# Optimization experiments

Hardware: AMD Instinct MI355X
Metric: run time of the kernel (lower is better)

Reference implementation:

```python
import jax, jax.numpy as jnp
import numpy as np

N_NODES = 25000
N_EDGES = 50000
NUM_ATOMS = 26
HID = 64
EMB = 64
N_GRAPHS = 64
NUM_NN_ITER = 3


def setup_inputs() -> dict:
    key = jax.random.key(0)
    ks = jax.random.split(key, 16)

    def nrm(k, shape, s=0.1):
        return jax.random.normal(k, shape, dtype=jnp.float32) * s

    x = jax.random.uniform(ks[0], (N_NODES, NUM_ATOMS), dtype=jnp.float32)
    edge_index = jax.random.randint(ks[1], (2, N_EDGES), 0, N_NODES)
    edge_attr = jax.random.uniform(ks[2], (N_EDGES, 4), dtype=jnp.float32)
    batch = jnp.sort(jax.random.randint(ks[3], (N_NODES,), 0, N_GRAPHS))

    params = dict(
        W_in=nrm(ks[4], (NUM_ATOMS, HID)), b_in=jnp.zeros((HID,), jnp.float32),
        We1=nrm(ks[5], (4, 128)), be1=jnp.zeros((128,), jnp.float32),
        We2=nrm(ks[6], (128, HID * HID), 0.02), be2=jnp.zeros((HID * HID,), jnp.float32),
        W_root=nrm(ks[7], (HID, HID)), b_conv=jnp.zeros((HID,), jnp.float32),
        W_ih=nrm(ks[8], (3 * HID, HID)), b_ih=jnp.zeros((3 * HID,), jnp.float32),
        W_hh=nrm(ks[9], (3 * HID, HID)), b_hh=jnp.zeros((3 * HID,), jnp.float32),
        Wo1=nrm(ks[10], (HID, HID)), bo1=jnp.zeros((HID,), jnp.float32),
        Wo2=nrm(ks[11], (HID, EMB)), bo2=jnp.zeros((EMB,), jnp.float32),
        Wp=nrm(ks[12], (EMB + NUM_ATOMS, 1)), bp=jnp.zeros((1,), jnp.float32),
    )
    return {"x": x, "edge_index": edge_index, "edge_attr": edge_attr, "batch": batch, **params}


def reference(x, edge_index, edge_attr, batch,
              W_in, b_in, We1, be1, We2, be2, W_root, b_conv,
              W_ih, b_ih, W_hh, b_hh, Wo1, bo1, Wo2, bo2, Wp, bp):
    src, dst = edge_index[0], edge_index[1]
    # edge MLP -> per-edge (HID, HID) weight blocks; edge_attr is fixed so compute once
    Wedge = (jax.nn.relu(edge_attr @ We1 + be1) @ We2 + be2).reshape(-1, HID, HID)  # (E, h, h)

    out = jax.nn.relu(x @ W_in + b_in)  # (N, h)
    h = out
    for _ in range(NUM_NN_ITER):
        # NNConv (aggr='add'): root transform + gather->bmm->scatter_add
        msg = jnp.einsum('ei,eio->eo', out[src], Wedge)           # (E, h)
        agg = jax.ops.segment_sum(msg, dst, num_segments=N_NODES)  # (N, h)
        m = jax.nn.relu(out @ W_root + agg + b_conv)
        # single-step GRU cell (torch GRU equations)
        gi = m @ W_ih.T + b_ih
        gh = h @ W_hh.T + b_hh
        i_r, i_z, i_n = jnp.split(gi, 3, axis=-1)
        h_r, h_z, h_n = jnp.split(gh, 3, axis=-1)
        r = jax.nn.sigmoid(i_r + h_r)
        z = jax.nn.sigmoid(i_z + h_z)
        n = jnp.tanh(i_n + r * h_n)
        h = (1.0 - z) * n + z * h
        out = h

    o = jax.nn.relu(out @ Wo1 + bo1) @ Wo2 + bo2            # (N, EMB)
    feat = jnp.concatenate([o, x], axis=1)                  # (N, EMB + NUM_ATOMS)
    # F.normalize: row-wise L2 with eps clamp
    feat = feat / jnp.maximum(jnp.linalg.norm(feat, axis=1, keepdims=True), 1e-12)
    # scatter_mean readout over graphs
    cnt = jax.ops.segment_sum(jnp.ones((N_NODES,), jnp.float32), batch, num_segments=N_GRAPHS)
    readout = jax.ops.segment_sum(feat, batch, num_segments=N_GRAPHS) / jnp.maximum(cnt, 1.0)[:, None]
    ratio = jax.nn.sigmoid(readout @ Wp + bp)               # (G, 1)
    return feat, ratio
```

## Files before the change

### kernel.cpp

```cpp
#include <hip/hip_runtime.h>
#include <math.h>

#define NN 25000
#define NE 50000
#define NEP2 50176
#define NBLK 196
#define NATOM 26
#define NUM_ITER 3
#define NCH 33
#define NPB 32

typedef __attribute__((ext_vector_type(8))) short bf16x8;
typedef __attribute__((ext_vector_type(8))) unsigned short ushort8_t;
typedef __attribute__((ext_vector_type(4))) float f32x4;
union FragU { bf16x8 v; ushort4 q[2]; };

static __device__ __forceinline__ ushort f2bf(float f) {
  unsigned u = __float_as_uint(f);
  unsigned r = (u + 0x7FFFu + ((u >> 16) & 1u)) >> 16;
  return (ushort)r;
}
static __device__ __forceinline__ unsigned cvt_pk_bf16(float a, float b) {
  unsigned r;
  asm("v_cvt_pk_bf16_f32 %0, %1, %2" : "=v"(r) : "v"(a), "v"(b));
  return r;
}
static __device__ __forceinline__ float bflo(unsigned u) { return __uint_as_float(u << 16); }
static __device__ __forceinline__ float bfhi(unsigned u) { return __uint_as_float(u & 0xFFFF0000u); }

__global__ __launch_bounds__(256) void edge_mlp_pack_kernel(
    const float* __restrict__ ea, const float* __restrict__ We1,
    const float* __restrict__ be1, ushort* __restrict__ Upkt) {
  int t = threadIdx.x;
  int el = t & 63, seg = t >> 6;
  int e = blockIdx.x * 64 + el;
  bool valid = (e < NE);
  float a0 = 0.f, a1 = 0.f, a2 = 0.f, a3 = 0.f;
  if (valid) { a0 = ea[e * 4]; a1 = ea[e * 4 + 1]; a2 = ea[e * 4 + 2]; a3 = ea[e * 4 + 3]; }
  #pragma unroll
  for (int q = 0; q < 8; ++q) {
    int g = seg * 8 + q;
    ushort out[4];
    #pragma unroll
    for (int kk = 0; kk < 4; ++kk) {
      int k = g * 4 + kk;
      float v = be1[k];
      v = fmaf(a0, We1[k], v);
      v = fmaf(a1, We1[128 + k], v);
      v = fmaf(a2, We1[256 + k], v);
      v = fmaf(a3, We1[384 + k], v);
      out[kk] = valid ? f2bf(fmaxf(v, 0.f)) : (ushort)0;
    }
    *(ushort4*)&Upkt[((size_t)g * NEP2 + e) * 4] = *(ushort4*)out;
  }
  if (seg == 0) {
    ushort out[4] = {(ushort)(valid ? 0x3F80 : 0), 0, 0, 0};
    *(ushort4*)&Upkt[((size_t)32 * NEP2 + e) * 4] = *(ushort4*)out;
  }
}

__global__ __launch_bounds__(256) void bpk_pack_kernel(
    const float* __restrict__ We2, const float* __restrict__ be2,
    ushort* __restrict__ Bpk) {
  int idx = blockIdx.x * 256 + threadIdx.x;
  int lane = idx & 63;
  int nt = (idx >> 6) & 3;
  int ks = (idx >> 8) & 7;
  int c = idx >> 11;
  int l15 = lane & 15, lg = lane >> 4;
  int o = nt * 16 + l15;
  ushort v[8];
  #pragma unroll
  for (int j = 0; j < 8; ++j) {
    int kl = (j < 4) ? (4 * lg + j) : (12 + 4 * lg + j);
    int f = c * 256 + ks * 32 + kl;
    int k = f >> 6, i = f & 63;
    float wv = 0.f;
    if (k < 128) wv = We2[(size_t)k * 4096 + i * 64 + o];
    else if (k == 128) wv = be2[i * 64 + o];
    v[j] = f2bf(wv);
  }
  *(ushort8_t*)(Bpk + (size_t)idx * 8) = *(ushort8_t*)v;
}

__global__ __launch_bounds__(256) void nw_pack_kernel(
    const float* __restrict__ W_root, const float* __restrict__ W_ih,
    const float* __restrict__ W_hh, ushort* __restrict__ Wr_pk,
    ushort* __restrict__ Bih_pk, ushort* __restrict__ Bhh_pk) {
  int idx = blockIdx.x * 256 + threadIdx.x;
  if (idx >= 3584) return;
  int lane, nt, ks, kind;
  ushort* dstp;
  if (idx < 512)      { kind = 0; int f = idx;        lane = f & 63; nt = (f >> 6) % 4;  ks = (f >> 6) / 4;  dstp = Wr_pk  + (size_t)f * 8; }
  else if (idx < 2048){ kind = 1; int f = idx - 512;  lane = f & 63; nt = (f >> 6) % 12; ks = (f >> 6) / 12; dstp = Bih_pk + (size_t)f * 8; }
  else                { kind = 2; int f = idx - 2048; lane = f & 63; nt = (f >> 6) % 12; ks = (f >> 6) / 12; dstp = Bhh_pk + (size_t)f * 8; }
  int l15 = lane & 15, lg = lane >> 4;
  int col = nt * 16 + l15;
  ushort v[8];
  #pragma unroll
  for (int j = 0; j < 8; ++j) {
    int kl = (j < 4) ? (4 * lg + j) : (12 + 4 * lg + j);
    int i = ks * 32 + kl;
    float wv;
    if (kind == 0)      wv = W_root[i * 64 + col];
    else if (kind == 1) wv = W_ih[col * 64 + i];
    else                wv = W_hh[col * 64 + i];
    v[j] = f2bf(wv);
  }
  *(ushort8_t*)dstp = *(ushort8_t*)v;
}

__global__ __launch_bounds__(512, 1) void edge_rgemm_kernel(
    const ushort* __restrict__ Upkt, const ushort* __restrict__ Bpk,
    const float* __restrict__ hv, const int* __restrict__ src,
    const int* __restrict__ dst, float* __restrict__ agg) {
  __shared__ ushort sB[2][16384];
  __shared__ ushort sU[2][1024];
  __shared__ ushort sS[256][72];
  int tid = threadIdx.x;
  int lane = tid & 63, w = tid >> 6;
  int l15 = lane & 15, lg = lane >> 4;
  int e0 = blockIdx.x * 256;

  #pragma unroll
  for (int r = 0; r < 8; ++r) {
    int idx = r * 512 + tid;
    int el = idx >> 4, part = idx & 15;
    int e = e0 + el;
    float4 v = make_float4(0.f, 0.f, 0.f, 0.f);
    if (e < NE) v = ((const float4*)hv)[(size_t)src[e] * 16 + part];
    unsigned lo = cvt_pk_bf16(v.x, v.y);
    unsigned hi = cvt_pk_bf16(v.z, v.w);
    *(uint2*)&sS[el][part * 4] = make_uint2(lo, hi);
  }

  ushort8_t rB[4]; uint2 rU;
  #pragma unroll
  for (int r = 0; r < 4; ++r)
    rB[r] = *(const ushort8_t*)(Bpk + ((size_t)r * 512 + tid) * 8);
  if (tid < 256) rU = *(const uint2*)(Upkt + (size_t)e0 * 4 + tid * 4);
  #pragma unroll
  for (int r = 0; r < 4; ++r)
    *(ushort8_t*)&sB[0][((size_t)r * 512 + tid) * 8] = rB[r];
  if (tid < 256) *(uint2*)&sU[0][tid * 4] = rU;
  __syncthreads();

  float4 sreg[2][2][2];
  #pragma unroll
  for (int mt = 0; mt < 2; ++mt)
    #pragma unroll
    for (int p = 0; p < 2; ++p)
      #pragma unroll
      for (int g = 0; g < 2; ++g) {
        uint2 d = *(const uint2*)&sS[w * 32 + mt * 16 + l15][p * 32 + g * 16 + 4 * lg];
        sreg[mt][p][g] = make_float4(bflo(d.x), bfhi(d.x), bflo(d.y), bfhi(d.y));
      }

  f32x4 acc[2][4];
  #pragma unroll
  for (int mt = 0; mt < 2; ++mt)
    #pragma unroll
    for (int nt = 0; nt < 4; ++nt) acc[mt][nt] = (f32x4){0.f, 0.f, 0.f, 0.f};

  for (int c = 0; c < NCH; ++c) {
    int cur = c & 1;
    bool more = (c + 1 < NCH);
    if (more) {
      const ushort* bs = Bpk + (size_t)(c + 1) * 16384;
      #pragma unroll
      for (int r = 0; r < 4; ++r)
        rB[r] = *(const ushort8_t*)(bs + ((size_t)r * 512 + tid) * 8);
      if (tid < 256)
        rU = *(const uint2*)(Upkt + ((size_t)(c + 1) * NEP2 + e0) * 4 + tid * 4);
    }
    float uu[2][4];
    #pragma unroll
    for (int mt = 0; mt < 2; ++mt) {
      uint2 d = *(const uint2*)&sU[cur][(w * 32 + mt * 16 + l15) * 4];
      uu[mt][0] = bflo(d.x); uu[mt][1] = bfhi(d.x);
      uu[mt][2] = bflo(d.y); uu[mt][3] = bfhi(d.y);
    }
    #pragma unroll
    for (int ks = 0; ks < 8; ++ks) {
      int p = ks & 1, ku = ks >> 1;
      bf16x8 bfr[4];
      #pragma unroll
      for (int nt = 0; nt < 4; ++nt)
        bfr[nt] = *(const bf16x8*)&sB[cur][(((size_t)ks * 4 + nt) * 64 + lane) * 8];
      #pragma unroll
      for (int mt = 0; mt < 2; ++mt) {
        float u = uu[mt][ku];
        float4 s0 = sreg[mt][p][0], s1 = sreg[mt][p][1];
        union { bf16x8 v; unsigned u32[4]; } af;
        af.u32[0] = cvt_pk_bf16(s0.x * u, s0.y * u);
        af.u32[1] = cvt_pk_bf16(s0.z * u, s0.w * u);
        af.u32[2] = cvt_pk_bf16(s1.x * u, s1.y * u);
        af.u32[3] = cvt_pk_bf16(s1.z * u, s1.w * u);
        #pragma unroll
        for (int nt = 0; nt < 4; ++nt)
          acc[mt][nt] = __builtin_amdgcn_mfma_f32_16x16x32_bf16(af.v, bfr[nt], acc[mt][nt], 0, 0, 0);
      }
    }
    if (more) {
      int nb = cur ^ 1;
      #pragma unroll
      for (int r = 0; r < 4; ++r)
        *(ushort8_t*)&sB[nb][((size_t)r * 512 + tid) * 8] = rB[r];
      if (tid < 256) *(uint2*)&sU[nb][tid * 4] = rU;
    }
    __syncthreads();
  }

  #pragma unroll
  for (int mt = 0; mt < 2; ++mt) {
    #pragma unroll
    for (int rr = 0; rr < 4; ++rr) {
      int e = e0 + w * 32 + mt * 16 + lg * 4 + rr;
      if (e < NE) {
        int d = dst[e];
        #pragma unroll
        for (int nt = 0; nt < 4; ++nt)
          atomicAdd(&agg[(size_t)d * 64 + nt * 16 + l15], acc[mt][nt][rr]);
      }
    }
  }
}

__global__ __launch_bounds__(256) void node_in_kernel(
    const float* __restrict__ x, const float* __restrict__ W_in,
    const float* __restrict__ b_in, float* __restrict__ h) {
  int idx = blockIdx.x * 256 + threadIdx.x;
  if (idx >= NN * 64) return;
  int n = idx >> 6, c = idx & 63;
  float acc = b_in[c];
  #pragma unroll
  for (int j = 0; j < NATOM; ++j) acc = fmaf(x[n * NATOM + j], W_in[j * 64 + c], acc);
  h[idx] = fmaxf(acc, 0.f);
}

__global__ __launch_bounds__(256, 1) void node_update2_kernel(
    float* __restrict__ hv, const float* __restrict__ agg,
    const ushort* __restrict__ Wr_pk, const ushort* __restrict__ Bih_pk,
    const ushort* __restrict__ Bhh_pk, const float* __restrict__ b_conv,
    const float* __restrict__ b_ih, const float* __restrict__ b_hh) {
  __shared__ ushort h_lds[128][72];
  __shared__ ushort m_lds[128][72];
  int tid = threadIdx.x;
  int lane = tid & 63, w = tid >> 6;
  int l15 = lane & 15, lg = lane >> 4;
  int n0 = blockIdx.x * 128;

  #pragma unroll
  for (int r = 0; r < 8; ++r) {
    int idx = r * 256 + tid;
    int row = idx >> 4, part = idx & 15;
    int n = n0 + row;
    float4 v = make_float4(0.f, 0.f, 0.f, 0.f);
    if (n < NN) v = ((const float4*)hv)[(size_t)n * 16 + part];
    *(uint2*)&h_lds[row][part * 4] =
        make_uint2(cvt_pk_bf16(v.x, v.y), cvt_pk_bf16(v.z, v.w));
  }
  __syncthreads();

  bf16x8 ah[2][2];
  #pragma unroll
  for (int mt = 0; mt < 2; ++mt)
    #pragma unroll
    for (int ks = 0; ks < 2; ++ks) {
      int row = w * 32 + mt * 16 + l15;
      FragU f;
      f.q[0] = *(const ushort4*)&h_lds[row][ks * 32 + 4 * lg];
      f.q[1] = *(const ushort4*)&h_lds[row][ks * 32 + 16 + 4 * lg];
      ah[mt][ks] = f.v;
    }

  f32x4 accm[2][4];
  #pragma unroll
  for (int mt = 0; mt < 2; ++mt)
    #pragma unroll
    for (int nt = 0; nt < 4; ++nt) accm[mt][nt] = (f32x4){0.f, 0.f, 0.f, 0.f};
  #pragma unroll
  for (int ks = 0; ks < 2; ++ks)
    #pragma unroll
    for (int nt = 0; nt < 4; ++nt) {
      bf16x8 b = *(const bf16x8*)(Wr_pk + ((size_t)((ks * 4 + nt) * 64 + lane)) * 8);
      #pragma unroll
      for (int mt = 0; mt < 2; ++mt)
        accm[mt][nt] = __builtin_amdgcn_mfma_f32_16x16x32_bf16(ah[mt][ks], b, accm[mt][nt], 0, 0, 0);
    }
  #pragma unroll
  for (int mt = 0; mt < 2; ++mt)
    #pragma unroll
    for (int nt = 0; nt < 4; ++nt) {
      int col = nt * 16 + l15;
      float bc = b_conv[col];
      #pragma unroll
      for (int rr = 0; rr < 4; ++rr) {
        int row = w * 32 + mt * 16 + lg * 4 + rr;
        int n = n0 + row;
        float val = 0.f;
        if (n < NN) val = fmaxf(accm[mt][nt][rr] + agg[(size_t)n * 64 + col] + bc, 0.f);
        m_lds[row][col] = f2bf(val);
      }
    }
  __syncthreads();

  bf16x8 am[2][2];
  #pragma unroll
  for (int mt = 0; mt < 2; ++mt)
    #pragma unroll
    for (int ks = 0; ks < 2; ++ks) {
      int row = w * 32 + mt * 16 + l15;
      FragU f;
      f.q[0] = *(const ushort4*)&m_lds[row][ks * 32 + 4 * lg];
      f.q[1] = *(const ushort4*)&m_lds[row][ks * 32 + 16 + 4 * lg];
      am[mt][ks] = f.v;
    }

  f32x4 acc_s[2][8], acc_in[2][4], acc_hn[2][4];
  #pragma unroll
  for (int mt = 0; mt < 2; ++mt) {
    #pragma unroll
    for (int nt = 0; nt < 8; ++nt) acc_s[mt][nt] = (f32x4){0.f, 0.f, 0.f, 0.f};
    #pragma unroll
    for (int nt = 0; nt < 4; ++nt) {
      acc_in[mt][nt] = (f32x4){0.f, 0.f, 0.f, 0.f};
      acc_hn[mt][nt] = (f32x4){0.f, 0.f, 0.f, 0.f};
    }
  }
  #pragma unroll
  for (int ks = 0; ks < 2; ++ks) {
    #pragma unroll
    for (int nt = 0; nt < 8; ++nt) {
      bf16x8 bi = *(const bf16x8*)(Bih_pk + ((size_t)((ks * 12 + nt) * 64 + lane)) * 8);
      bf16x8 bh = *(const bf16x8*)(Bhh_pk + ((size_t)((ks * 12 + nt) * 64 + lane)) * 8);
      #pragma unroll
      for (int mt = 0; mt < 2; ++mt) {
        acc_s[mt][nt] = __builtin_amdgcn_mfma_f32_16x16x32_bf16(am[mt][ks], bi, acc_s[mt][nt], 0, 0, 0);
        acc_s[mt][nt] = __builtin_amdgcn_mfma_f32_16x16x32_bf16(ah[mt][ks], bh, acc_s[mt][nt], 0, 0, 0);
      }
    }
    #pragma unroll
    for (int nt = 8; nt < 12; ++nt) {
      bf16x8 bi = *(const bf16x8*)(Bih_pk + ((size_t)((ks * 12 + nt) * 64 + lane)) * 8);
      bf16x8 bh = *(const bf16x8*)(Bhh_pk + ((size_t)((ks * 12 + nt) * 64 + lane)) * 8);
      #pragma unroll
      for (int mt = 0; mt < 2; ++mt) {
        acc_in[mt][nt - 8] = __builtin_amdgcn_mfma_f32_16x16x32_bf16(am[mt][ks], bi, acc_in[mt][nt - 8], 0, 0, 0);
        acc_hn[mt][nt - 8] = __builtin_amdgcn_mfma_f32_16x16x32_bf16(ah[mt][ks], bh, acc_hn[mt][nt - 8], 0, 0, 0);
      }
    }
  }

  #pragma unroll
  for (int mt = 0; mt < 2; ++mt)
    #pragma unroll
    for (int nt = 0; nt < 4; ++nt) {
      int col = nt * 16 + l15;
      float b_sr = b_ih[col] + b_hh[col];
      float b_sz = b_ih[64 + col] + b_hh[64 + col];
      float b_in_ = b_ih[128 + col];
      float b_hn = b_hh[128 + col];
      #pragma unroll
      for (int rr = 0; rr < 4; ++rr) {
        int row = w * 32 + mt * 16 + lg * 4 + rr;
        int n = n0 + row;
        if (n >= NN) continue;
        float Sr = acc_s[mt][nt][rr] + b_sr;
        float Sz = acc_s[mt][nt + 4][rr] + b_sz;
        float vin = acc_in[mt][nt][rr] + b_in_;
        float vhn = acc_hn[mt][nt][rr] + b_hn;
        float r = 1.f / (1.f + __expf(-Sr));
        float z = 1.f / (1.f + __expf(-Sz));
        float nn = tanhf(fmaf(r, vhn, vin));
        float hp = hv[(size_t)n * 64 + col];
        hv[(size_t)n * 64 + col] = (1.f - z) * nn + z * hp;
      }
    }
}

__global__ __launch_bounds__(256) void head2_kernel(
    const float* __restrict__ hv, const float* __restrict__ x,
    const float* __restrict__ Wo1, const float* __restrict__ bo1,
    const float* __restrict__ Wo2, const float* __restrict__ bo2,
    float* __restrict__ feat) {
  __shared__ float wo1[64 * 64];
  __shared__ float wo2[64 * 64];
  __shared__ float s_row[NPB * 64];
  __shared__ float s_o1[NPB * 64];
  int tid = threadIdx.x;
  int n0 = blockIdx.x * NPB;

  for (int idx = tid; idx < 64 * 16; idx += 256) {
    ((float4*)wo1)[idx] = ((const float4*)Wo1)[idx];
    ((float4*)wo2)[idx] = ((const float4*)Wo2)[idx];
  }
  for (int idx = tid; idx < NPB * 64; idx += 256) {
    int n = n0 + (idx >> 6);
    s_row[idx] = (n < NN) ? hv[(size_t)n * 64 + (idx & 63)] : 0.f;
  }
  __syncthreads();

  int c = tid & 63, g = tid >> 6;
  #pragma unroll
  for (int q = 0; q < 8; ++q) {
    int nl = g + 4 * q;
    float a = bo1[c];
    for (int i = 0; i < 64; ++i) a = fmaf(s_row[nl * 64 + i], wo1[i * 64 + c], a);
    s_o1[nl * 64 + c] = fmaxf(a, 0.f);
  }
  __syncthreads();
  #pragma unroll
  for (int q = 0; q < 8; ++q) {
    int nl = g + 4 * q;
    int n = n0 + nl;
    float b = bo2[c];
    for (int i = 0; i < 64; ++i) b = fmaf(s_o1[nl * 64 + i], wo2[i * 64 + c], b);
    float xv = (c < NATOM && n < NN) ? x[(size_t)n * NATOM + c] : 0.f;
    float sq = b * b + xv * xv;
    #pragma unroll
    for (int off = 1; off < 64; off <<= 1) sq += __shfl_xor(sq, off);
    if (n >= NN) continue;
    float inv = 1.f / fmaxf(sqrtf(sq), 1e-12f);
    feat[(size_t)n * 90 + c] = b * inv;
    if (c < NATOM) feat[(size_t)n * 90 + 64 + c] = xv * inv;
  }
}

static __device__ __forceinline__ int lbound(const int* __restrict__ b, int v) {
  int lo = 0, hi = NN;
  while (lo < hi) { int m = (lo + hi) >> 1; if (b[m] < v) lo = m + 1; else hi = m; }
  return lo;
}

__global__ __launch_bounds__(128) void readout_kernel(
    const float* __restrict__ feat, const int* __restrict__ batch,
    float* __restrict__ readout, float* __restrict__ cnt) {
  __shared__ int bounds[2];
  int g = blockIdx.x;
  int t = threadIdx.x;
  if (t == 0) bounds[0] = lbound(batch, g);
  if (t == 1) bounds[1] = lbound(batch, g + 1);
  __syncthreads();
  int lo = bounds[0], hi = bounds[1];
  if (t < 90) {
    float a0 = 0.f, a1 = 0.f, a2 = 0.f, a3 = 0.f;
    int n = lo;
    for (; n + 3 < hi; n += 4) {
      a0 += feat[(size_t)n * 90 + t];
      a1 += feat[(size_t)(n + 1) * 90 + t];
      a2 += feat[(size_t)(n + 2) * 90 + t];
      a3 += feat[(size_t)(n + 3) * 90 + t];
    }
    for (; n < hi; ++n) a0 += feat[(size_t)n * 90 + t];
    readout[g * 90 + t] = (a0 + a1) + (a2 + a3);
  }
  if (t == 0) cnt[g] = (float)(hi - lo);
}

__global__ __launch_bounds__(64) void ratio_kernel(
    const float* __restrict__ readout, const float* __restrict__ cnt,
    const float* __restrict__ Wp, const float* __restrict__ bp,
    float* __restrict__ ratio) {
  int g = threadIdx.x;
  float c = fmaxf(cnt[g], 1.f);
  float a = bp[0];
  for (int j = 0; j < 90; ++j) a = fmaf(readout[g * 90 + j] / c, Wp[j], a);
  ratio[g] = 1.f / (1.f + __expf(-a));
}


extern "C" void kernel_launch(void* const* d_in, const int* in_sizes, int n_in,
                              void* d_out, int out_size, void* d_ws, size_t ws_size,
                              hipStream_t stream) {
  const float* x      = (const float*)d_in[0];
  const int*   ei     = (const int*)  d_in[1];
  const float* ea     = (const float*)d_in[2];
  const int*   batch  = (const int*)  d_in[3];
  const float* W_in   = (const float*)d_in[4];
  const float* b_in   = (const float*)d_in[5];
  const float* We1    = (const float*)d_in[6];
  const float* be1    = (const float*)d_in[7];
  const float* We2    = (const float*)d_in[8];
  const float* be2    = (const float*)d_in[9];
  const float* W_root = (const float*)d_in[10];
  const float* b_conv = (const float*)d_in[11];
  const float* W_ih   = (const float*)d_in[12];
  const float* b_ih   = (const float*)d_in[13];
  const float* W_hh   = (const float*)d_in[14];
  const float* b_hh   = (const float*)d_in[15];
  const float* Wo1    = (const float*)d_in[16];
  const float* bo1    = (const float*)d_in[17];
  const float* Wo2    = (const float*)d_in[18];
  const float* bo2    = (const float*)d_in[19];
  const float* Wp     = (const float*)d_in[20];
  const float* bp     = (const float*)d_in[21];

  const int* srcp = ei;
  const int* dstp = ei + NE;
  float* feat  = (float*)d_out;
  float* ratio = feat + (size_t)NN * 90;

  char* wsb = (char*)d_ws;
  ushort* Upkt   = (ushort*)(wsb + 0);
  ushort* Bpk    = (ushort*)(wsb + 13246464);
  float*  h      = (float*) (wsb + 14327808);
  float*  agg    = (float*) (wsb + 20727808);
  float*  readout= (float*) (wsb + 27127808);
  float*  cnt    = (float*) (wsb + 27150848);
  ushort* Wr_pk  = (ushort*)(wsb + 27151104);
  ushort* Bih_pk = (ushort*)(wsb + 27159296);
  ushort* Bhh_pk = (ushort*)(wsb + 27183872);

  edge_mlp_pack_kernel<<<NEP2 / 64, 256, 0, stream>>>(ea, We1, be1, Upkt);
  bpk_pack_kernel<<<(NCH * 8 * 4 * 64) / 256, 256, 0, stream>>>(We2, be2, Bpk);
  nw_pack_kernel<<<14, 256, 0, stream>>>(W_root, W_ih, W_hh, Wr_pk, Bih_pk, Bhh_pk);
  node_in_kernel<<<(NN * 64 + 255) / 256, 256, 0, stream>>>(x, W_in, b_in, h);

  for (int it = 0; it < NUM_ITER; ++it) {
    hipMemsetAsync(agg, 0, (size_t)NN * 64 * sizeof(float), stream);
    edge_rgemm_kernel<<<NBLK, 512, 0, stream>>>(Upkt, Bpk, h, srcp, dstp, agg);
    node_update2_kernel<<<(NN + 127) / 128, 256, 0, stream>>>(
        h, agg, Wr_pk, Bih_pk, Bhh_pk, b_conv, b_ih, b_hh);
  }

  head2_kernel<<<(NN + NPB - 1) / NPB, 256, 0, stream>>>(
      h, x, Wo1, bo1, Wo2, bo2, feat);
  readout_kernel<<<64, 128, 0, stream>>>(feat, batch, readout, cnt);
  ratio_kernel<<<1, 64, 0, stream>>>(readout, cnt, Wp, bp, ratio);
}
```

Before: 423.9 us.

## Double edge tile per block and split chunk reduction across two grid slices

```diff
diff --git a/kernel.cpp b/kernel.cpp
--- a/kernel.cpp
+++ b/kernel.cpp
@@ -4,11 +4,12 @@
 #define NN 25000
 #define NE 50000
 #define NEP2 50176
-#define NBLK 196
 #define NATOM 26
 #define NUM_ITER 3
 #define NCH 33
 #define NPB 32
+#define EB2 512
+#define KSP 17
 
 typedef __attribute__((ext_vector_type(8))) short bf16x8;
 typedef __attribute__((ext_vector_type(8))) unsigned short ushort8_t;
@@ -110,20 +111,22 @@
   *(ushort8_t*)dstp = *(ushort8_t*)v;
 }
 
-__global__ __launch_bounds__(512, 1) void edge_rgemm_kernel(
+__global__ __launch_bounds__(512, 2) void edge_rgemm2_kernel(
     const ushort* __restrict__ Upkt, const ushort* __restrict__ Bpk,
     const float* __restrict__ hv, const int* __restrict__ src,
     const int* __restrict__ dst, float* __restrict__ agg) {
   __shared__ ushort sB[2][16384];
-  __shared__ ushort sU[2][1024];
-  __shared__ ushort sS[256][72];
+  __shared__ ushort sU[2][2048];
+  __shared__ ushort sS[512][72];
   int tid = threadIdx.x;
   int lane = tid & 63, w = tid >> 6;
   int l15 = lane & 15, lg = lane >> 4;
-  int e0 = blockIdx.x * 256;
-
-  #pragma unroll
-  for (int r = 0; r < 8; ++r) {
+  int e0 = blockIdx.x * EB2;
+  int c0 = blockIdx.y * KSP;
+  int c1 = (c0 + KSP < NCH) ? (c0 + KSP) : NCH;
+
+  #pragma unroll
+  for (int r = 0; r < 16; ++r) {
     int idx = r * 512 + tid;
     int el = idx >> 4, part = idx & 15;
     int e = e0 + el;
@@ -135,48 +138,50 @@
   }
 
   ushort8_t rB[4]; uint2 rU;
-  #pragma unroll
-  for (int r = 0; r < 4; ++r)
-    rB[r] = *(const ushort8_t*)(Bpk + ((size_t)r * 512 + tid) * 8);
-  if (tid < 256) rU = *(const uint2*)(Upkt + (size_t)e0 * 4 + tid * 4);
+  {
+    const ushort* bs = Bpk + (size_t)c0 * 16384;
+    #pragma unroll
+    for (int r = 0; r < 4; ++r)
+      rB[r] = *(const ushort8_t*)(bs + ((size_t)r * 512 + tid) * 8);
+    rU = *(const uint2*)(Upkt + ((size_t)c0 * NEP2 + e0) * 4 + tid * 4);
+  }
   #pragma unroll
   for (int r = 0; r < 4; ++r)
     *(ushort8_t*)&sB[0][((size_t)r * 512 + tid) * 8] = rB[r];
-  if (tid < 256) *(uint2*)&sU[0][tid * 4] = rU;
+  *(uint2*)&sU[0][tid * 4] = rU;
   __syncthreads();
 
-  float4 sreg[2][2][2];
-  #pragma unroll
-  for (int mt = 0; mt < 2; ++mt)
+  float4 sreg[4][2][2];
+  #pragma unroll
+  for (int mt = 0; mt < 4; ++mt)
     #pragma unroll
     for (int p = 0; p < 2; ++p)
       #pragma unroll
       for (int g = 0; g < 2; ++g) {
-        uint2 d = *(const uint2*)&sS[w * 32 + mt * 16 + l15][p * 32 + g * 16 + 4 * lg];
+        uint2 d = *(const uint2*)&sS[w * 64 + mt * 16 + l15][p * 32 + g * 16 + 4 * lg];
         sreg[mt][p][g] = make_float4(bflo(d.x), bfhi(d.x), bflo(d.y), bfhi(d.y));
       }
 
-  f32x4 acc[2][4];
-  #pragma unroll
-  for (int mt = 0; mt < 2; ++mt)
+  f32x4 acc[4][4];
+  #pragma unroll
+  for (int mt = 0; mt < 4; ++mt)
     #pragma unroll
     for (int nt = 0; nt < 4; ++nt) acc[mt][nt] = (f32x4){0.f, 0.f, 0.f, 0.f};
 
-  for (int c = 0; c < NCH; ++c) {
-    int cur = c & 1;
-    bool more = (c + 1 < NCH);
+  for (int c = c0; c < c1; ++c) {
+    int cur = (c - c0) & 1;
+    bool more = (c + 1 < c1);
     if (more) {
       const ushort* bs = Bpk + (size_t)(c + 1) * 16384;
       #pragma unroll
       for (int r = 0; r < 4; ++r)
         rB[r] = *(const ushort8_t*)(bs + ((size_t)r * 512 + tid) * 8);
-      if (tid < 256)
-        rU = *(const uint2*)(Upkt + ((size_t)(c + 1) * NEP2 + e0) * 4 + tid * 4);
-    }
-    float uu[2][4];
-    #pragma unroll
-    for (int mt = 0; mt < 2; ++mt) {
-      uint2 d = *(const uint2*)&sU[cur][(w * 32 + mt * 16 + l15) * 4];
+      rU = *(const uint2*)(Upkt + ((size_t)(c + 1) * NEP2 + e0) * 4 + tid * 4);
+    }
+    float uu[4][4];
+    #pragma unroll
+    for (int mt = 0; mt < 4; ++mt) {
+      uint2 d = *(const uint2*)&sU[cur][(w * 64 + mt * 16 + l15) * 4];
       uu[mt][0] = bflo(d.x); uu[mt][1] = bfhi(d.x);
       uu[mt][2] = bflo(d.y); uu[mt][3] = bfhi(d.y);
     }
@@ -188,7 +193,7 @@
       for (int nt = 0; nt < 4; ++nt)
         bfr[nt] = *(const bf16x8*)&sB[cur][(((size_t)ks * 4 + nt) * 64 + lane) * 8];
       #pragma unroll
-      for (int mt = 0; mt < 2; ++mt) {
+      for (int mt = 0; mt < 4; ++mt) {
         float u = uu[mt][ku];
         float4 s0 = sreg[mt][p][0], s1 = sreg[mt][p][1];
         union { bf16x8 v; unsigned u32[4]; } af;
@@ -206,16 +211,16 @@
       #pragma unroll
       for (int r = 0; r < 4; ++r)
         *(ushort8_t*)&sB[nb][((size_t)r * 512 + tid) * 8] = rB[r];
-      if (tid < 256) *(uint2*)&sU[nb][tid * 4] = rU;
+      *(uint2*)&sU[nb][tid * 4] = rU;
     }
     __syncthreads();
   }
 
   #pragma unroll
-  for (int mt = 0; mt < 2; ++mt) {
+  for (int mt = 0; mt < 4; ++mt) {
     #pragma unroll
     for (int rr = 0; rr < 4; ++rr) {
-      int e = e0 + w * 32 + mt * 16 + lg * 4 + rr;
+      int e = e0 + w * 64 + mt * 16 + lg * 4 + rr;
       if (e < NE) {
         int d = dst[e];
         #pragma unroll
@@ -519,7 +524,8 @@
 
   for (int it = 0; it < NUM_ITER; ++it) {
     hipMemsetAsync(agg, 0, (size_t)NN * 64 * sizeof(float), stream);
-    edge_rgemm_kernel<<<NBLK, 512, 0, stream>>>(Upkt, Bpk, h, srcp, dstp, agg);
+    edge_rgemm2_kernel<<<dim3(NEP2 / EB2, 2), 512, 0, stream>>>(
+        Upkt, Bpk, h, srcp, dstp, agg);
     node_update2_kernel<<<(NN + 127) / 128, 256, 0, stream>>>(
         h, agg, Wr_pk, Bih_pk, Bhh_pk, b_conv, b_ih, b_hh);
   }
```

Result: slower. 441.6 us (+4.2%).
